# Performance work log

Hardware: AMD Instinct MI355X
Metric: run time of the kernel (lower is better)

Reference implementation:

```python
import jax, jax.numpy as jnp
import numpy as np

TEMPERATURE = 0.5
EPS = 1e-8  # matches F.cosine_similarity eps clamp


def setup_inputs() -> dict:
    key = jax.random.key(0)
    k1, k2 = jax.random.split(key)
    logits = jax.random.normal(k1, (8192, 256), dtype=jnp.float32)
    label = jax.random.randint(k2, (8192,), 0, 10, dtype=jnp.int64)
    return {"logits": logits, "label": label}


def reference(logits, label):
    n = label.shape[0]
    # pairwise cosine similarity via normalize + GEMM (same math as the
    # broadcasted F.cosine_similarity, without the O(n^2 d) intermediate)
    norms = jnp.maximum(jnp.linalg.norm(logits, axis=1, keepdims=True), EPS)
    xn = logits / norms                       # [n, d]
    sim_matrix = xn @ xn.T                    # [n, n]

    eye = jnp.eye(n, dtype=sim_matrix.dtype)
    mask = (label[:, None] == label[None, :]).astype(sim_matrix.dtype)  # same-label (incl. diag)

    e = jnp.exp(sim_matrix / TEMPERATURE) * (1.0 - eye)  # zero diagonal
    sim = mask * e                            # same-label positives
    no_sim_sum = jnp.sum(e - sim, axis=1)     # [n] row sums of different-label terms
    sim_sum = sim + no_sim_sum[:, None]       # denominator per entry
    ratio = sim / sim_sum

    # zeros (different-label entries) get +1 via (1 - mask), diagonal gets +1 via eye -> -log(1) = 0
    loss_mat = -jnp.log((1.0 - mask) + ratio + eye)
    return jnp.sum(loss_mat) / (2 * n)
```

## Files before the change

### kernel.cpp

```cpp
#include <hip/hip_runtime.h>
#include <cstdint>
#include <cstddef>

typedef float  f32x4  __attribute__((ext_vector_type(4)));
typedef long long i64;
typedef unsigned char uchar;

#define N_ROWS 8192
#define KDIM   256
#define TEMP_INV 2.0f
#define LOG2E  1.4426950408889634f
#define EXPC   (TEMP_INV * LOG2E)

__global__ __launch_bounds__(1024) void build_perm(const int* __restrict__ label,
        int* __restrict__ perm, int* __restrict__ labelPerm,
        int* __restrict__ classStart, int* __restrict__ cumTiles)
{
    __shared__ unsigned short lcnt[1024][10];
    __shared__ int cstart[11];
    __shared__ int ccount[10];
    const int tid = threadIdx.x;
    const int wave = tid >> 6, lane = tid & 63;

    int lab[8];
    #pragma unroll
    for (int j = 0; j < 8; ++j) {
        int c = label[tid + j * 1024];
        lab[j] = (c < 0) ? 0 : (c > 9 ? 9 : c);
    }
    unsigned short loc[10] = {0,0,0,0,0,0,0,0,0,0};
    #pragma unroll
    for (int j = 0; j < 8; ++j) loc[lab[j]]++;
    #pragma unroll
    for (int c = 0; c < 10; ++c) lcnt[tid][c] = loc[c];
    __syncthreads();

    if (wave < 10) {
        const int c = wave;
        int s[16]; int tot = 0;
        #pragma unroll
        for (int m = 0; m < 16; ++m) { s[m] = lcnt[lane * 16 + m][c]; tot += s[m]; }
        int incl = tot;
        #pragma unroll
        for (int d = 1; d < 64; d <<= 1) {
            int up = __shfl_up(incl, d, 64);
            if (lane >= d) incl += up;
        }
        int run = incl - tot;
        #pragma unroll
        for (int m = 0; m < 16; ++m) { lcnt[lane * 16 + m][c] = (unsigned short)run; run += s[m]; }
        if (lane == 63) ccount[c] = incl;
    }
    __syncthreads();

    if (tid == 0) {
        int run = 0, runT = 0;
        for (int c = 0; c < 10; ++c) {
            cstart[c] = run; classStart[c] = run;
            int tpc = (ccount[c] + 127) >> 7;
            cumTiles[c] = runT;
            run  += ccount[c];
            runT += tpc * (tpc + 1) / 2;
        }
        cstart[10] = run; classStart[10] = run; cumTiles[10] = runT;
    }
    __syncthreads();

    int ofs[10];
    #pragma unroll
    for (int c = 0; c < 10; ++c) ofs[c] = lcnt[tid][c];
    #pragma unroll
    for (int j = 0; j < 8; ++j) {
        int c = lab[j];
        int pos = cstart[c] + ofs[c]++;
        perm[pos] = tid + j * 1024;
        labelPerm[pos] = c;
    }
}

__global__ __launch_bounds__(256) void normalize_rows(const float* __restrict__ logits,
        const int* __restrict__ perm, uchar* __restrict__ xn8)
{
    const int p = blockIdx.x * 4 + (threadIdx.x >> 6);
    const int lane = threadIdx.x & 63;
    const int old = perm[p];
    float4 v = reinterpret_cast<const float4*>(logits + (size_t)old * KDIM)[lane];
    float ss = v.x*v.x + v.y*v.y + v.z*v.z + v.w*v.w;
    #pragma unroll
    for (int off = 32; off >= 1; off >>= 1) ss += __shfl_xor(ss, off, 64);
    float inv = 1.0f / fmaxf(sqrtf(ss), 1e-8f);
    float x0 = v.x * inv, x1 = v.y * inv, x2 = v.z * inv, x3 = v.w * inv;
    int pk = __builtin_amdgcn_cvt_pk_fp8_f32(x0, x1, 0, false);
    pk     = __builtin_amdgcn_cvt_pk_fp8_f32(x2, x3, pk, true);
    reinterpret_cast<unsigned int*>(xn8 + (size_t)p * KDIM)[lane] = (unsigned int)pk;
}

__device__ __forceinline__ void stage_pair_fp8(const uchar* __restrict__ xn8,
        int rowBase, int colBase, int kb, uchar* As, uchar* Bs, int wave, int lane)
{
    #pragma unroll
    for (int it = 0; it < 2; ++it) {
        int ci = it * 256 + wave * 64 + lane;
        int row = ci >> 2;
        int c = (ci & 3) ^ (row & 3);
        const uchar* gA = xn8 + (size_t)(rowBase + row) * KDIM + kb + c * 16;
        const uchar* gB = xn8 + (size_t)(colBase + row) * KDIM + kb + c * 16;
        uchar* lA = As + (size_t)ci * 16;
        uchar* lB = Bs + (size_t)ci * 16;
        __builtin_amdgcn_global_load_lds((const __attribute__((address_space(1))) void*)gA,
                                         (__attribute__((address_space(3))) void*)lA, 16, 0, 0);
        __builtin_amdgcn_global_load_lds((const __attribute__((address_space(1))) void*)gB,
                                         (__attribute__((address_space(3))) void*)lB, 16, 0, 0);
    }
}

__device__ __forceinline__ void read_frags8(const uchar* As, const uchar* Bs,
        i64 (&a)[2][4], i64 (&b)[2][4], int wave, int lane)
{
    const int wr = wave >> 1, wc = wave & 1;
    const int lrow = lane & 15, kgrp = lane >> 4;
    const int ch = kgrp >> 1, half = kgrp & 1;
    #pragma unroll
    for (int kk = 0; kk < 2; ++kk) {
        const int c16 = kk * 2 + ch;
        #pragma unroll
        for (int mi = 0; mi < 4; ++mi) {
            const int row = wr*64 + mi*16 + lrow;
            a[kk][mi] = *reinterpret_cast<const i64*>(As + (size_t)row * 64 + ((c16 ^ (row & 3)) * 16) + half * 8);
        }
        #pragma unroll
        for (int ni = 0; ni < 4; ++ni) {
            const int row = wc*64 + ni*16 + lrow;
            b[kk][ni] = *reinterpret_cast<const i64*>(Bs + (size_t)row * 64 + ((c16 ^ (row & 3)) * 16) + half * 8);
        }
    }
}

__device__ __forceinline__ void mfma_frags8(i64 (&a)[2][4], i64 (&b)[2][4], f32x4 (&acc)[4][4])
{
    #pragma unroll
    for (int kk = 0; kk < 2; ++kk)
        #pragma unroll
        for (int mi = 0; mi < 4; ++mi)
            #pragma unroll
            for (int ni = 0; ni < 4; ++ni)
                acc[mi][ni] = __builtin_amdgcn_mfma_f32_16x16x32_fp8_fp8(a[kk][mi], b[kk][ni], acc[mi][ni], 0, 0, 0);
}

#define PIPE8_READS_RELEASE(Ac, Bc)                                  \
    i64 a[2][4], b[2][4];                                            \
    read_frags8(Ac, Bc, a, b, wave, lane);                           \
    __builtin_amdgcn_sched_barrier(0);                               \
    asm volatile("s_waitcnt lgkmcnt(0)" ::: "memory");               \
    __builtin_amdgcn_sched_barrier(0);                               \
    __builtin_amdgcn_s_barrier();                                    \
    __builtin_amdgcn_sched_barrier(0);

#define PIPE8_MFMA()                                                 \
    __builtin_amdgcn_s_setprio(1);                                   \
    mfma_frags8(a, b, acc);                                          \
    __builtin_amdgcn_s_setprio(0);

#define PIPE8_TAIL(N)                                                \
    __builtin_amdgcn_sched_barrier(0);                               \
    asm volatile("s_waitcnt vmcnt(" #N ")" ::: "memory");            \
    __builtin_amdgcn_s_barrier();                                    \
    __builtin_amdgcn_sched_barrier(0);

__device__ __forceinline__ void kloop_fp8(const uchar* __restrict__ xn8,
        int rowBase, int colBase, f32x4 (&acc)[4][4],
        uchar* As0, uchar* Bs0, uchar* As1, uchar* Bs1, int wave, int lane)
{
    stage_pair_fp8(xn8, rowBase, colBase, 0,  As0, Bs0, wave, lane);
    stage_pair_fp8(xn8, rowBase, colBase, 64, As1, Bs1, wave, lane);
    asm volatile("s_waitcnt vmcnt(4)" ::: "memory");
    __builtin_amdgcn_s_barrier();
    __builtin_amdgcn_sched_barrier(0);
    {
        PIPE8_READS_RELEASE(As0, Bs0)
        stage_pair_fp8(xn8, rowBase, colBase, 128, As0, Bs0, wave, lane);
        PIPE8_MFMA()
        PIPE8_TAIL(4)
    }
    {
        PIPE8_READS_RELEASE(As1, Bs1)
        stage_pair_fp8(xn8, rowBase, colBase, 192, As1, Bs1, wave, lane);
        PIPE8_MFMA()
        PIPE8_TAIL(4)
    }
    {
        PIPE8_READS_RELEASE(As0, Bs0)
        PIPE8_MFMA()
        PIPE8_TAIL(0)
    }
    {
        PIPE8_READS_RELEASE(As1, Bs1)
        PIPE8_MFMA()
    }
}

__global__ __launch_bounds__(256, 4) void phase1_gemm(const uchar* __restrict__ xn8,
        const int* __restrict__ labelPerm, float* __restrict__ pD)
{
    __shared__ __align__(16) char pool[32768];
    uchar* As0 = (uchar*)(pool);
    uchar* Bs0 = (uchar*)(pool + 8192);
    uchar* As1 = (uchar*)(pool + 16384);
    uchar* Bs1 = (uchar*)(pool + 24576);
    float* rowD = (float*)pool;
    float* colD = (float*)(pool + 16384);
    __shared__ int labLDS[256];

    const int tid = threadIdx.x;
    const int wave = tid >> 6, lane = tid & 63;

    int t = blockIdx.x, bi = 0;
    while (t >= 64 - bi) { t -= 64 - bi; ++bi; }
    const int bj = bi + t;
    const bool isDiag = (bi == bj);
    const int rowBase = bi * 128, colBase = bj * 128;

    if (labelPerm[rowBase] == labelPerm[colBase + 127]) {
        if (tid < 128)       pD[(size_t)bj * N_ROWS + rowBase + tid] = 0.f;
        else if (!isDiag)    pD[(size_t)bi * N_ROWS + colBase + tid - 128] = 0.f;
        return;
    }

    labLDS[tid] = labelPerm[(tid < 128) ? (rowBase + tid) : (colBase + tid - 128)];
    __builtin_amdgcn_sched_barrier(0);

    f32x4 acc[4][4] = {};
    kloop_fp8(xn8, rowBase, colBase, acc, As0, Bs0, As1, Bs1, wave, lane);

    const int wr = wave >> 1, wc = wave & 1;
    const int lrow = lane & 15, lgrp = lane >> 4;
    float colAcc[4] = {0.f, 0.f, 0.f, 0.f};
    #pragma unroll
    for (int mi = 0; mi < 4; ++mi) {
        #pragma unroll
        for (int reg = 0; reg < 4; ++reg) {
            const int tr = wr * 64 + mi * 16 + lgrp * 4 + reg;
            const int rl = labLDS[tr];
            float rowAcc = 0.f;
            #pragma unroll
            for (int ni = 0; ni < 4; ++ni) {
                const int tc = wc * 64 + ni * 16 + lrow;
                float e = __builtin_amdgcn_exp2f(acc[mi][ni][reg] * EXPC);
                float ed = (rl != labLDS[128 + tc]) ? e : 0.f;
                rowAcc += ed;
                colAcc[ni] += ed;
            }
            rowD[tr * 32 + wc * 16 + lrow] = rowAcc;
        }
    }
    if (!isDiag) {
        #pragma unroll
        for (int ni = 0; ni < 4; ++ni) {
            const int tc = wc * 64 + ni * 16 + lrow;
            colD[tc * 8 + wr * 4 + lgrp] = colAcc[ni];
        }
    }
    __syncthreads();

    if (tid < 128) {
        const float* p = rowD + tid * 32;
        float s = 0.f;
        #pragma unroll
        for (int k = 0; k < 8; ++k) {
            f32x4 v = *reinterpret_cast<const f32x4*>(p + k * 4);
            s += v[0] + v[1] + v[2] + v[3];
        }
        pD[(size_t)bj * N_ROWS + rowBase + tid] = s;
    } else if (!isDiag) {
        const int c2 = tid - 128;
        const float* p = colD + c2 * 8;
        f32x4 v0 = *reinterpret_cast<const f32x4*>(p);
        f32x4 v1 = *reinterpret_cast<const f32x4*>(p + 4);
        pD[(size_t)bi * N_ROWS + colBase + c2] =
            v0[0] + v0[1] + v0[2] + v0[3] + v1[0] + v1[1] + v1[2] + v1[3];
    }
}

__global__ __launch_bounds__(256, 4) void phase3_loss(const uchar* __restrict__ xn8,
        const float* __restrict__ pD, const int* __restrict__ classStart,
        const int* __restrict__ cumTiles, float* __restrict__ partial)
{
    __shared__ __align__(16) char pool[32768];
    uchar* As0 = (uchar*)(pool);
    uchar* Bs0 = (uchar*)(pool + 8192);
    uchar* As1 = (uchar*)(pool + 16384);
    uchar* Bs1 = (uchar*)(pool + 24576);
    __shared__ float redF[256];
    __shared__ float DarrH[256];
    __shared__ float DarrR[128];
    __shared__ float DarrC[128];
    __shared__ int   meta[22];

    const int tid = threadIdx.x;
    const int wave = tid >> 6, lane = tid & 63;
    const int b = blockIdx.x;

    if (tid < 11) { meta[tid] = classStart[tid]; meta[11 + tid] = cumTiles[tid]; }
    __syncthreads();
    const int nTiles = meta[11 + 10];
    if (b >= nTiles) return;

    int c = 0;
    while (c < 9 && b >= meta[11 + c + 1]) ++c;
    const int s = meta[c], e = meta[c + 1];
    const int nc = e - s;
    const int tps = (nc + 127) >> 7;
    int lt = b - meta[11 + c];
    int ti = 0;
    while (lt >= tps - ti) { lt -= tps - ti; ++ti; }
    const int tj = ti + lt;
    const bool isDiagT = (ti == tj);
    const int rowBase = s + ti * 128, colBase = s + tj * 128;

    {
        int r = rowBase + (tid & 127); if (r > N_ROWS - 1) r = N_ROWS - 1;
        const int half = tid >> 7;
        float d = 0.f;
        #pragma unroll 4
        for (int sl = half * 32; sl < half * 32 + 32; ++sl)
            d += pD[(size_t)sl * N_ROWS + r];
        DarrH[(tid & 127) * 2 + half] = d;
    }
    __syncthreads();
    if (tid < 128) DarrR[tid] = DarrH[tid * 2] + DarrH[tid * 2 + 1];
    __syncthreads();
    if (!isDiagT) {
        int r = colBase + (tid & 127); if (r > N_ROWS - 1) r = N_ROWS - 1;
        const int half = tid >> 7;
        float d = 0.f;
        #pragma unroll 4
        for (int sl = half * 32; sl < half * 32 + 32; ++sl)
            d += pD[(size_t)sl * N_ROWS + r];
        DarrH[(tid & 127) * 2 + half] = d;
        __syncthreads();
        if (tid < 128) DarrC[tid] = DarrH[tid * 2] + DarrH[tid * 2 + 1];
    }
    asm volatile("s_waitcnt vmcnt(0)" ::: "memory");
    __syncthreads();

    f32x4 acc[4][4] = {};
    kloop_fp8(xn8, rowBase, colBase, acc, As0, Bs0, As1, Bs1, wave, lane);

    const int wr = wave >> 1, wc = wave & 1;
    const int lrow = lane & 15, lgrp = lane >> 4;
    float lsum = 0.f;
    #pragma unroll
    for (int mi = 0; mi < 4; ++mi) {
        #pragma unroll
        for (int reg = 0; reg < 4; ++reg) {
            const int tr = wr * 64 + mi * 16 + lgrp * 4 + reg;
            const int r = rowBase + tr;
            if (r < e) {
                const float Dr = DarrR[tr];
                #pragma unroll
                for (int ni = 0; ni < 4; ++ni) {
                    const int tc = wc * 64 + ni * 16 + lrow;
                    const int cg = colBase + tc;
                    if (cg < e) {
                        float sim = acc[mi][ni][reg];
                        float ev = __builtin_amdgcn_exp2f(sim * EXPC);
                        if (isDiagT) {
                            if (cg != r)
                                lsum += __logf(ev + Dr) - TEMP_INV * sim;
                        } else {
                            lsum += __logf(ev + Dr) + __logf(ev + DarrC[tc])
                                  - 2.0f * TEMP_INV * sim;
                        }
                    }
                }
            }
        }
    }
    redF[tid] = lsum;
    __syncthreads();
    for (int st = 128; st > 0; st >>= 1) {
        if (tid < st) redF[tid] += redF[tid + st];
        __syncthreads();
    }
    if (tid == 0) partial[b] = redF[0];
}

__global__ void phase4_final(const float* __restrict__ partial, const int* __restrict__ cumTiles,
                             float* __restrict__ out)
{
    __shared__ float red[256];
    const int tid = threadIdx.x;
    const int nTiles = cumTiles[10];
    float s = 0.f;
    for (int i = tid; i < nTiles; i += 256) s += partial[i];
    red[tid] = s;
    __syncthreads();
    for (int st = 128; st > 0; st >>= 1) {
        if (tid < st) red[tid] += red[tid + st];
        __syncthreads();
    }
    if (tid == 0) out[0] = red[0] * (1.0f / 16384.0f);
}

extern "C" void kernel_launch(void* const* d_in, const int* in_sizes, int n_in,
                              void* d_out, int out_size, void* d_ws, size_t ws_size,
                              hipStream_t stream)
{
    const float* logits = (const float*)d_in[0];
    const int*   label  = (const int*)d_in[1];
    float* out = (float*)d_out;

    char* ws = (char*)d_ws;
    uchar*  xn8       = (uchar*)(ws);
    float*  pD        = (float*)(ws + (2u << 20));
    int*    perm      = (int*)(ws + (4u << 20));
    int*    labelPerm = (int*)(ws + (4u << 20) + (32u << 10));
    int*    classStart= (int*)(ws + (4u << 20) + (64u << 10));
    int*    cumTiles  = (int*)(ws + (4u << 20) + (64u << 10) + 256);
    float*  partial   = (float*)(ws + (4u << 20) + (128u << 10));

    hipLaunchKernelGGL(build_perm, dim3(1), dim3(1024), 0, stream,
                       label, perm, labelPerm, classStart, cumTiles);
    hipLaunchKernelGGL(normalize_rows, dim3(2048), dim3(256), 0, stream,
                       logits, perm, xn8);
    hipLaunchKernelGGL(phase1_gemm, dim3(2080), dim3(256), 0, stream,
                       xn8, labelPerm, pD);
    hipLaunchKernelGGL(phase3_loss, dim3(2080), dim3(256), 0, stream,
                       xn8, pD, classStart, cumTiles, partial);
    hipLaunchKernelGGL(phase4_final, dim3(1), dim3(256), 0, stream,
                       partial, cumTiles, out);
}
```

Before: 73.09 us.

## Fuse perm build with normalization, gather rows via perm, persistent loss kernel

Merges the label-permutation kernel and the row-normalization kernel into one launch. Rows are now normalized in original order, and the GEMM staging loads gather through perm, which removes the dependency of normalization on the permutation. The loss kernel becomes a persistent grid of 512 blocks that loop over tiles, and the final reduction reads exactly 512 partials. The cost is indirect, gathered global loads in the GEMM, plus a permutation build that now runs in a single block on 256 threads with serial loops.

```diff
diff --git a/kernel.cpp b/kernel.cpp
--- a/kernel.cpp
+++ b/kernel.cpp
@@ -12,43 +12,60 @@
 #define LOG2E  1.4426950408889634f
 #define EXPC   (TEMP_INV * LOG2E)
 
-__global__ __launch_bounds__(1024) void build_perm(const int* __restrict__ label,
+#define AS1 __attribute__((address_space(1)))
+#define AS3 __attribute__((address_space(3)))
+
+__global__ __launch_bounds__(256) void prep(const float* __restrict__ logits,
+        const int* __restrict__ label, uchar* __restrict__ xn8,
         int* __restrict__ perm, int* __restrict__ labelPerm,
         int* __restrict__ classStart, int* __restrict__ cumTiles)
 {
-    __shared__ unsigned short lcnt[1024][10];
+    __shared__ int lcnt[256][10];
     __shared__ int cstart[11];
     __shared__ int ccount[10];
     const int tid = threadIdx.x;
+    const int bid = blockIdx.x;
+
+    if (bid < 2048) {
+        const int p = bid * 4 + (tid >> 6);
+        const int lane = tid & 63;
+        float4 v = reinterpret_cast<const float4*>(logits + (size_t)p * KDIM)[lane];
+        float ss = v.x*v.x + v.y*v.y + v.z*v.z + v.w*v.w;
+        #pragma unroll
+        for (int off = 32; off >= 1; off >>= 1) ss += __shfl_xor(ss, off, 64);
+        float inv = 1.0f / fmaxf(sqrtf(ss), 1e-8f);
+        int pk = __builtin_amdgcn_cvt_pk_fp8_f32(v.x * inv, v.y * inv, 0, false);
+        pk     = __builtin_amdgcn_cvt_pk_fp8_f32(v.z * inv, v.w * inv, pk, true);
+        reinterpret_cast<unsigned int*>(xn8 + (size_t)p * KDIM)[lane] = (unsigned int)pk;
+        return;
+    }
+
     const int wave = tid >> 6, lane = tid & 63;
-
-    int lab[8];
-    #pragma unroll
-    for (int j = 0; j < 8; ++j) {
-        int c = label[tid + j * 1024];
-        lab[j] = (c < 0) ? 0 : (c > 9 ? 9 : c);
-    }
-    unsigned short loc[10] = {0,0,0,0,0,0,0,0,0,0};
-    #pragma unroll
-    for (int j = 0; j < 8; ++j) loc[lab[j]]++;
+    const int beg = tid * 32, end = beg + 32;
+    int loc[10] = {0,0,0,0,0,0,0,0,0,0};
+    for (int i = beg; i < end; ++i) {
+        int c = label[i]; c = (c < 0) ? 0 : (c > 9 ? 9 : c);
+        loc[c]++;
+    }
     #pragma unroll
     for (int c = 0; c < 10; ++c) lcnt[tid][c] = loc[c];
     __syncthreads();
 
-    if (wave < 10) {
-        const int c = wave;
-        int s[16]; int tot = 0;
-        #pragma unroll
-        for (int m = 0; m < 16; ++m) { s[m] = lcnt[lane * 16 + m][c]; tot += s[m]; }
+    for (int c = wave; c < 10; c += 4) {
+        int s0 = lcnt[lane*4+0][c], s1 = lcnt[lane*4+1][c];
+        int s2 = lcnt[lane*4+2][c], s3 = lcnt[lane*4+3][c];
+        int tot = s0 + s1 + s2 + s3;
         int incl = tot;
         #pragma unroll
         for (int d = 1; d < 64; d <<= 1) {
             int up = __shfl_up(incl, d, 64);
             if (lane >= d) incl += up;
         }
-        int run = incl - tot;
-        #pragma unroll
-        for (int m = 0; m < 16; ++m) { lcnt[lane * 16 + m][c] = (unsigned short)run; run += s[m]; }
+        int excl = incl - tot;
+        lcnt[lane*4+0][c] = excl;
+        lcnt[lane*4+1][c] = excl + s0;
+        lcnt[lane*4+2][c] = excl + s0 + s1;
+        lcnt[lane*4+3][c] = excl + s0 + s1 + s2;
         if (lane == 63) ccount[c] = incl;
     }
     __syncthreads();
@@ -69,49 +86,22 @@
     int ofs[10];
     #pragma unroll
     for (int c = 0; c < 10; ++c) ofs[c] = lcnt[tid][c];
-    #pragma unroll
-    for (int j = 0; j < 8; ++j) {
-        int c = lab[j];
+    for (int i = beg; i < end; ++i) {
+        int c = label[i]; c = (c < 0) ? 0 : (c > 9 ? 9 : c);
         int pos = cstart[c] + ofs[c]++;
-        perm[pos] = tid + j * 1024;
+        perm[pos] = i;
         labelPerm[pos] = c;
     }
 }
 
-__global__ __launch_bounds__(256) void normalize_rows(const float* __restrict__ logits,
-        const int* __restrict__ perm, uchar* __restrict__ xn8)
-{
-    const int p = blockIdx.x * 4 + (threadIdx.x >> 6);
-    const int lane = threadIdx.x & 63;
-    const int old = perm[p];
-    float4 v = reinterpret_cast<const float4*>(logits + (size_t)old * KDIM)[lane];
-    float ss = v.x*v.x + v.y*v.y + v.z*v.z + v.w*v.w;
-    #pragma unroll
-    for (int off = 32; off >= 1; off >>= 1) ss += __shfl_xor(ss, off, 64);
-    float inv = 1.0f / fmaxf(sqrtf(ss), 1e-8f);
-    float x0 = v.x * inv, x1 = v.y * inv, x2 = v.z * inv, x3 = v.w * inv;
-    int pk = __builtin_amdgcn_cvt_pk_fp8_f32(x0, x1, 0, false);
-    pk     = __builtin_amdgcn_cvt_pk_fp8_f32(x2, x3, pk, true);
-    reinterpret_cast<unsigned int*>(xn8 + (size_t)p * KDIM)[lane] = (unsigned int)pk;
-}
-
-__device__ __forceinline__ void stage_pair_fp8(const uchar* __restrict__ xn8,
-        int rowBase, int colBase, int kb, uchar* As, uchar* Bs, int wave, int lane)
-{
-    #pragma unroll
-    for (int it = 0; it < 2; ++it) {
-        int ci = it * 256 + wave * 64 + lane;
-        int row = ci >> 2;
-        int c = (ci & 3) ^ (row & 3);
-        const uchar* gA = xn8 + (size_t)(rowBase + row) * KDIM + kb + c * 16;
-        const uchar* gB = xn8 + (size_t)(colBase + row) * KDIM + kb + c * 16;
-        uchar* lA = As + (size_t)ci * 16;
-        uchar* lB = Bs + (size_t)ci * 16;
-        __builtin_amdgcn_global_load_lds((const __attribute__((address_space(1))) void*)gA,
-                                         (__attribute__((address_space(3))) void*)lA, 16, 0, 0);
-        __builtin_amdgcn_global_load_lds((const __attribute__((address_space(1))) void*)gB,
-                                         (__attribute__((address_space(3))) void*)lB, 16, 0, 0);
-    }
+__device__ __forceinline__ void stage2(const uchar* sA0, const uchar* sA1,
+        const uchar* sB0, const uchar* sB1, int kb,
+        uchar* As, uchar* Bs, int lo0, int lo1)
+{
+    __builtin_amdgcn_global_load_lds((const AS1 void*)(sA0 + kb), (AS3 void*)(As + lo0), 16, 0, 0);
+    __builtin_amdgcn_global_load_lds((const AS1 void*)(sA1 + kb), (AS3 void*)(As + lo1), 16, 0, 0);
+    __builtin_amdgcn_global_load_lds((const AS1 void*)(sB0 + kb), (AS3 void*)(Bs + lo0), 16, 0, 0);
+    __builtin_amdgcn_global_load_lds((const AS1 void*)(sB1 + kb), (AS3 void*)(Bs + lo1), 16, 0, 0);
 }
 
 __device__ __forceinline__ void read_frags8(const uchar* As, const uchar* Bs,
@@ -167,40 +157,47 @@
     __builtin_amdgcn_s_barrier();                                    \
     __builtin_amdgcn_sched_barrier(0);
 
-__device__ __forceinline__ void kloop_fp8(const uchar* __restrict__ xn8,
-        int rowBase, int colBase, f32x4 (&acc)[4][4],
-        uchar* As0, uchar* Bs0, uchar* As1, uchar* Bs1, int wave, int lane)
-{
-    stage_pair_fp8(xn8, rowBase, colBase, 0,  As0, Bs0, wave, lane);
-    stage_pair_fp8(xn8, rowBase, colBase, 64, As1, Bs1, wave, lane);
-    asm volatile("s_waitcnt vmcnt(4)" ::: "memory");
-    __builtin_amdgcn_s_barrier();
-    __builtin_amdgcn_sched_barrier(0);
-    {
-        PIPE8_READS_RELEASE(As0, Bs0)
-        stage_pair_fp8(xn8, rowBase, colBase, 128, As0, Bs0, wave, lane);
-        PIPE8_MFMA()
-        PIPE8_TAIL(4)
-    }
-    {
-        PIPE8_READS_RELEASE(As1, Bs1)
-        stage_pair_fp8(xn8, rowBase, colBase, 192, As1, Bs1, wave, lane);
-        PIPE8_MFMA()
-        PIPE8_TAIL(4)
-    }
-    {
-        PIPE8_READS_RELEASE(As0, Bs0)
-        PIPE8_MFMA()
-        PIPE8_TAIL(0)
-    }
-    {
-        PIPE8_READS_RELEASE(As1, Bs1)
-        PIPE8_MFMA()
-    }
-}
+#define KLOOP_FP8()                                                           \
+    stage2(sA0, sA1, sB0, sB1, 0,   As0, Bs0, lo0, lo1);                      \
+    stage2(sA0, sA1, sB0, sB1, 64,  As1, Bs1, lo0, lo1);                      \
+    asm volatile("s_waitcnt vmcnt(4)" ::: "memory");                          \
+    __builtin_amdgcn_s_barrier();                                             \
+    __builtin_amdgcn_sched_barrier(0);                                        \
+    {                                                                         \
+        PIPE8_READS_RELEASE(As0, Bs0)                                         \
+        stage2(sA0, sA1, sB0, sB1, 128, As0, Bs0, lo0, lo1);                  \
+        PIPE8_MFMA()                                                          \
+        PIPE8_TAIL(4)                                                         \
+    }                                                                         \
+    {                                                                         \
+        PIPE8_READS_RELEASE(As1, Bs1)                                         \
+        stage2(sA0, sA1, sB0, sB1, 192, As1, Bs1, lo0, lo1);                  \
+        PIPE8_MFMA()                                                          \
+        PIPE8_TAIL(4)                                                         \
+    }                                                                         \
+    {                                                                         \
+        PIPE8_READS_RELEASE(As0, Bs0)                                         \
+        PIPE8_MFMA()                                                          \
+        PIPE8_TAIL(0)                                                         \
+    }                                                                         \
+    {                                                                         \
+        PIPE8_READS_RELEASE(As1, Bs1)                                         \
+        PIPE8_MFMA()                                                          \
+    }
+
+#define TILE_SRC_SETUP(rowBase, colBase)                                      \
+    const int ci0 = wave * 64 + lane, ci1 = 256 + wave * 64 + lane;           \
+    const int r0 = ci0 >> 2, r1 = ci1 >> 2;                                   \
+    const int c0 = (ci0 & 3) ^ (r0 & 3), c1 = (ci1 & 3) ^ (r1 & 3);           \
+    const uchar* sA0 = xn8 + (size_t)perm[(rowBase) + r0] * KDIM + c0 * 16;   \
+    const uchar* sA1 = xn8 + (size_t)perm[(rowBase) + r1] * KDIM + c1 * 16;   \
+    const uchar* sB0 = xn8 + (size_t)perm[(colBase) + r0] * KDIM + c0 * 16;   \
+    const uchar* sB1 = xn8 + (size_t)perm[(colBase) + r1] * KDIM + c1 * 16;   \
+    const int lo0 = ci0 * 16, lo1 = ci1 * 16;
 
 __global__ __launch_bounds__(256, 4) void phase1_gemm(const uchar* __restrict__ xn8,
-        const int* __restrict__ labelPerm, float* __restrict__ pD)
+        const int* __restrict__ perm, const int* __restrict__ labelPerm,
+        float* __restrict__ pD)
 {
     __shared__ __align__(16) char pool[32768];
     uchar* As0 = (uchar*)(pool);
@@ -227,10 +224,11 @@
     }
 
     labLDS[tid] = labelPerm[(tid < 128) ? (rowBase + tid) : (colBase + tid - 128)];
+    TILE_SRC_SETUP(rowBase, colBase)
     __builtin_amdgcn_sched_barrier(0);
 
     f32x4 acc[4][4] = {};
-    kloop_fp8(xn8, rowBase, colBase, acc, As0, Bs0, As1, Bs1, wave, lane);
+    KLOOP_FP8()
 
     const int wr = wave >> 1, wc = wave & 1;
     const int lrow = lane & 15, lgrp = lane >> 4;
@@ -282,8 +280,9 @@
 }
 
 __global__ __launch_bounds__(256, 4) void phase3_loss(const uchar* __restrict__ xn8,
-        const float* __restrict__ pD, const int* __restrict__ classStart,
-        const int* __restrict__ cumTiles, float* __restrict__ partial)
+        const int* __restrict__ perm, const float* __restrict__ pD,
+        const int* __restrict__ classStart, const int* __restrict__ cumTiles,
+        float* __restrict__ partial)
 {
     __shared__ __align__(16) char pool[32768];
     uchar* As0 = (uchar*)(pool);
@@ -298,101 +297,104 @@
 
     const int tid = threadIdx.x;
     const int wave = tid >> 6, lane = tid & 63;
-    const int b = blockIdx.x;
 
     if (tid < 11) { meta[tid] = classStart[tid]; meta[11 + tid] = cumTiles[tid]; }
     __syncthreads();
     const int nTiles = meta[11 + 10];
-    if (b >= nTiles) return;
-
-    int c = 0;
-    while (c < 9 && b >= meta[11 + c + 1]) ++c;
-    const int s = meta[c], e = meta[c + 1];
-    const int nc = e - s;
-    const int tps = (nc + 127) >> 7;
-    int lt = b - meta[11 + c];
-    int ti = 0;
-    while (lt >= tps - ti) { lt -= tps - ti; ++ti; }
-    const int tj = ti + lt;
-    const bool isDiagT = (ti == tj);
-    const int rowBase = s + ti * 128, colBase = s + tj * 128;
-
-    {
-        int r = rowBase + (tid & 127); if (r > N_ROWS - 1) r = N_ROWS - 1;
-        const int half = tid >> 7;
-        float d = 0.f;
-        #pragma unroll 4
-        for (int sl = half * 32; sl < half * 32 + 32; ++sl)
-            d += pD[(size_t)sl * N_ROWS + r];
-        DarrH[(tid & 127) * 2 + half] = d;
-    }
-    __syncthreads();
-    if (tid < 128) DarrR[tid] = DarrH[tid * 2] + DarrH[tid * 2 + 1];
-    __syncthreads();
-    if (!isDiagT) {
-        int r = colBase + (tid & 127); if (r > N_ROWS - 1) r = N_ROWS - 1;
-        const int half = tid >> 7;
-        float d = 0.f;
-        #pragma unroll 4
-        for (int sl = half * 32; sl < half * 32 + 32; ++sl)
-            d += pD[(size_t)sl * N_ROWS + r];
-        DarrH[(tid & 127) * 2 + half] = d;
-        __syncthreads();
-        if (tid < 128) DarrC[tid] = DarrH[tid * 2] + DarrH[tid * 2 + 1];
-    }
-    asm volatile("s_waitcnt vmcnt(0)" ::: "memory");
-    __syncthreads();
-
-    f32x4 acc[4][4] = {};
-    kloop_fp8(xn8, rowBase, colBase, acc, As0, Bs0, As1, Bs1, wave, lane);
-
-    const int wr = wave >> 1, wc = wave & 1;
-    const int lrow = lane & 15, lgrp = lane >> 4;
-    float lsum = 0.f;
-    #pragma unroll
-    for (int mi = 0; mi < 4; ++mi) {
-        #pragma unroll
-        for (int reg = 0; reg < 4; ++reg) {
-            const int tr = wr * 64 + mi * 16 + lgrp * 4 + reg;
-            const int r = rowBase + tr;
-            if (r < e) {
-                const float Dr = DarrR[tr];
-                #pragma unroll
-                for (int ni = 0; ni < 4; ++ni) {
-                    const int tc = wc * 64 + ni * 16 + lrow;
-                    const int cg = colBase + tc;
-                    if (cg < e) {
-                        float sim = acc[mi][ni][reg];
-                        float ev = __builtin_amdgcn_exp2f(sim * EXPC);
-                        if (isDiagT) {
-                            if (cg != r)
-                                lsum += __logf(ev + Dr) - TEMP_INV * sim;
-                        } else {
-                            lsum += __logf(ev + Dr) + __logf(ev + DarrC[tc])
-                                  - 2.0f * TEMP_INV * sim;
+
+    float tileSum = 0.f;
+    for (int b = blockIdx.x; b < nTiles; b += 512) {
+        __syncthreads();
+
+        int c = 0;
+        while (c < 9 && b >= meta[11 + c + 1]) ++c;
+        const int s = meta[c], e = meta[c + 1];
+        const int nc = e - s;
+        const int tps = (nc + 127) >> 7;
+        int lt = b - meta[11 + c];
+        int ti = 0;
+        while (lt >= tps - ti) { lt -= tps - ti; ++ti; }
+        const int tj = ti + lt;
+        const bool isDiagT = (ti == tj);
+        const int rowBase = s + ti * 128, colBase = s + tj * 128;
+
+        {
+            int r = rowBase + (tid & 127); if (r > N_ROWS - 1) r = N_ROWS - 1;
+            const int half = tid >> 7;
+            float d = 0.f;
+            #pragma unroll 4
+            for (int sl = half * 32; sl < half * 32 + 32; ++sl)
+                d += pD[(size_t)sl * N_ROWS + r];
+            DarrH[(tid & 127) * 2 + half] = d;
+        }
+        __syncthreads();
+        if (tid < 128) DarrR[tid] = DarrH[tid * 2] + DarrH[tid * 2 + 1];
+        __syncthreads();
+        if (!isDiagT) {
+            int r = colBase + (tid & 127); if (r > N_ROWS - 1) r = N_ROWS - 1;
+            const int half = tid >> 7;
+            float d = 0.f;
+            #pragma unroll 4
+            for (int sl = half * 32; sl < half * 32 + 32; ++sl)
+                d += pD[(size_t)sl * N_ROWS + r];
+            DarrH[(tid & 127) * 2 + half] = d;
+            __syncthreads();
+            if (tid < 128) DarrC[tid] = DarrH[tid * 2] + DarrH[tid * 2 + 1];
+        }
+
+        TILE_SRC_SETUP(rowBase, colBase)
+        asm volatile("s_waitcnt vmcnt(0)" ::: "memory");
+        __syncthreads();
+
+        f32x4 acc[4][4] = {};
+        KLOOP_FP8()
+
+        const int wr = wave >> 1, wc = wave & 1;
+        const int lrow = lane & 15, lgrp = lane >> 4;
+        #pragma unroll
+        for (int mi = 0; mi < 4; ++mi) {
+            #pragma unroll
+            for (int reg = 0; reg < 4; ++reg) {
+                const int tr = wr * 64 + mi * 16 + lgrp * 4 + reg;
+                const int r = rowBase + tr;
+                if (r < e) {
+                    const float Dr = DarrR[tr];
+                    #pragma unroll
+                    for (int ni = 0; ni < 4; ++ni) {
+                        const int tc = wc * 64 + ni * 16 + lrow;
+                        const int cg = colBase + tc;
+                        if (cg < e) {
+                            float sim = acc[mi][ni][reg];
+                            float ev = __builtin_amdgcn_exp2f(sim * EXPC);
+                            if (isDiagT) {
+                                if (cg != r)
+                                    tileSum += __logf(ev + Dr) - TEMP_INV * sim;
+                            } else {
+                                tileSum += __logf(ev + Dr) + __logf(ev + DarrC[tc])
+                                         - 2.0f * TEMP_INV * sim;
+                            }
                         }
                     }
                 }
             }
         }
     }
-    redF[tid] = lsum;
+
+    __syncthreads();
+    redF[tid] = tileSum;
     __syncthreads();
     for (int st = 128; st > 0; st >>= 1) {
         if (tid < st) redF[tid] += redF[tid + st];
         __syncthreads();
     }
-    if (tid == 0) partial[b] = redF[0];
-}
-
-__global__ void phase4_final(const float* __restrict__ partial, const int* __restrict__ cumTiles,
-                             float* __restrict__ out)
+    if (tid == 0) partial[blockIdx.x] = redF[0];
+}
+
+__global__ void phase4_final(const float* __restrict__ partial, float* __restrict__ out)
 {
     __shared__ float red[256];
     const int tid = threadIdx.x;
-    const int nTiles = cumTiles[10];
-    float s = 0.f;
-    for (int i = tid; i < nTiles; i += 256) s += partial[i];
+    float s = partial[tid] + partial[tid + 256];
     red[tid] = s;
     __syncthreads();
     for (int st = 128; st > 0; st >>= 1) {
@@ -419,14 +421,12 @@
     int*    cumTiles  = (int*)(ws + (4u << 20) + (64u << 10) + 256);
     float*  partial   = (float*)(ws + (4u << 20) + (128u << 10));
 
-    hipLaunchKernelGGL(build_perm, dim3(1), dim3(1024), 0, stream,
-                       label, perm, labelPerm, classStart, cumTiles);
-    hipLaunchKernelGGL(normalize_rows, dim3(2048), dim3(256), 0, stream,
-                       logits, perm, xn8);
+    hipLaunchKernelGGL(prep, dim3(2049), dim3(256), 0, stream,
+                       logits, label, xn8, perm, labelPerm, classStart, cumTiles);
     hipLaunchKernelGGL(phase1_gemm, dim3(2080), dim3(256), 0, stream,
-                       xn8, labelPerm, pD);
-    hipLaunchKernelGGL(phase3_loss, dim3(2080), dim3(256), 0, stream,
-                       xn8, pD, classStart, cumTiles, partial);
+                       xn8, perm, labelPerm, pD);
+    hipLaunchKernelGGL(phase3_loss, dim3(512), dim3(256), 0, stream,
+                       xn8, perm, pD, classStart, cumTiles, partial);
     hipLaunchKernelGGL(phase4_final, dim3(1), dim3(256), 0, stream,
-                       partial, cumTiles, out);
-}
+                       partial, out);
+}
```

After: 72.37 us. About the same (-1.0%).
